# Performance work log

Measured on AMD Instinct MI355X. Metric: run time of the kernel, lower is better.

The kernel has to match this reference:

```python
import jax, jax.numpy as jnp
import numpy as np

TROPICAL_ZERO = jnp.float32(-1e38)  # tropical additive identity (acts as -inf)


def setup_inputs() -> dict:
    key = jax.random.key(0)
    k_x, k_w = jax.random.split(key)
    B, IN, OUT = 4096, 256, 256
    x = jax.random.normal(k_x, (B, IN), dtype=jnp.float32)
    # weight = log(rand + 1e-6), matching nn.Parameter init in the torch module
    weight = jnp.log(jax.random.uniform(k_w, (OUT, IN), dtype=jnp.float32) + 1e-6)
    bias = jnp.zeros((OUT,), dtype=jnp.float32)
    return {"x": x, "weight": weight, "bias": bias}


def reference(x, weight, bias):
    # Tropical (max-plus) matmul: out[b, j] = max_k (x[b, k] + w[j, k]) + bias[j]
    # restricted to 'non-tropical-zero' products; if all products are tropical
    # zero, the output stays TROPICAL_ZERO (no bias added), as in the torch loop.
    products = x[:, None, :] + weight[None, :, :]          # [B, out, in]
    mask = products > TROPICAL_ZERO                        # [B, out, in]
    masked = jnp.where(mask, products, -jnp.inf)
    max_val = jnp.max(masked, axis=-1)                     # [B, out]
    any_valid = jnp.any(mask, axis=-1)                     # [B, out]
    out = jnp.where(any_valid, max_val + bias[None, :], TROPICAL_ZERO)
    return out
```

## Files before the change

kernel.cpp:

```cpp
#include <hip/hip_runtime.h>


#define TZERO -1e38f

constexpr int Bdim = 4096;
constexpr int K    = 256;
constexpr int N    = 256;
constexpr int BM   = 64;
constexpr int BN   = 32;
constexpr int BK   = 32;
constexpr int XLD  = BM + 4;
constexpr int WLD  = BN + 4;
constexpr int NT   = 128;

__global__ __launch_bounds__(NT)
void tropical_kernel(const float* __restrict__ x, const float* __restrict__ w,
                     const float* __restrict__ bias, float* __restrict__ out)
{
    __shared__ float xs[BK][XLD];
    __shared__ float ws[BK][WLD];

    const int t    = threadIdx.x;
    const int tx   = t & 15;
    const int ty   = t >> 4;
    const int row0 = blockIdx.x * BM;
    const int col0 = blockIdx.y * BN;

    float acc[4][4];
#pragma unroll
    for (int i = 0; i < 4; ++i)
#pragma unroll
        for (int j = 0; j < 4; ++j)
            acc[i][j] = -__builtin_inff();

    for (int kc = 0; kc < K; kc += BK) {
#pragma unroll
        for (int i = 0; i < 4; ++i) {
            const int f  = t + i * NT;
            const int r  = f >> 3;
            const int k4 = f & 7;
            const float4 v = *reinterpret_cast<const float4*>(
                &x[(size_t)(row0 + r) * K + kc + k4 * 4]);
            xs[k4 * 4 + 0][r] = v.x;
            xs[k4 * 4 + 1][r] = v.y;
            xs[k4 * 4 + 2][r] = v.z;
            xs[k4 * 4 + 3][r] = v.w;
        }
#pragma unroll
        for (int i = 0; i < 2; ++i) {
            const int f  = t + i * NT;
            const int c  = f >> 3;
            const int k4 = f & 7;
            const float4 v = *reinterpret_cast<const float4*>(
                &w[(size_t)(col0 + c) * K + kc + k4 * 4]);
            ws[k4 * 4 + 0][c] = v.x;
            ws[k4 * 4 + 1][c] = v.y;
            ws[k4 * 4 + 2][c] = v.z;
            ws[k4 * 4 + 3][c] = v.w;
        }
        __syncthreads();

#pragma unroll
        for (int k = 0; k < BK; k += 2) {
            float xa[4], xb[4], wa[4], wb[4];
            *reinterpret_cast<float4*>(xa) =
                *reinterpret_cast<const float4*>(&xs[k][tx * 4]);
            *reinterpret_cast<float4*>(xb) =
                *reinterpret_cast<const float4*>(&xs[k + 1][tx * 4]);
            *reinterpret_cast<float4*>(wa) =
                *reinterpret_cast<const float4*>(&ws[k][ty * 4]);
            *reinterpret_cast<float4*>(wb) =
                *reinterpret_cast<const float4*>(&ws[k + 1][ty * 4]);
#pragma unroll
            for (int i = 0; i < 4; ++i)
#pragma unroll
                for (int j = 0; j < 4; ++j) {
                    const float t0 = xa[i] + wa[j];
                    const float t1 = xb[i] + wb[j];
                    acc[i][j] = fmaxf(fmaxf(acc[i][j], t0), t1);
                }
        }
        __syncthreads();
    }

    float bj[4];
    *reinterpret_cast<float4*>(bj) =
        *reinterpret_cast<const float4*>(&bias[col0 + ty * 4]);
#pragma unroll
    for (int i = 0; i < 4; ++i) {
        float4 o;
        o.x = (acc[i][0] > TZERO) ? acc[i][0] + bj[0] : TZERO;
        o.y = (acc[i][1] > TZERO) ? acc[i][1] + bj[1] : TZERO;
        o.z = (acc[i][2] > TZERO) ? acc[i][2] + bj[2] : TZERO;
        o.w = (acc[i][3] > TZERO) ? acc[i][3] + bj[3] : TZERO;
        *reinterpret_cast<float4*>(
            &out[(size_t)(row0 + tx * 4 + i) * N + col0 + ty * 4]) = o;
    }
}

extern "C" void kernel_launch(void* const* d_in, const int* in_sizes, int n_in,
                              void* d_out, int out_size, void* d_ws, size_t ws_size,
                              hipStream_t stream) {
    const float* x  = (const float*)d_in[0];
    const float* w  = (const float*)d_in[1];
    const float* b  = (const float*)d_in[2];
    float* out      = (float*)d_out;

    dim3 grid(Bdim / BM, N / BN);
    tropical_kernel<<<grid, NT, 0, stream>>>(x, w, b, out);
}
```

Measured before the change: 87.08 us.

## Restructure tropical matmul: full-K weight tile in LDS, x rows broadcast from global

Each block now stages a full 64-column by 256-K weight tile in shared memory as float4, and each wave handles 8 batch rows with one output column per lane. The x values are read straight from global memory with wave-uniform addresses, so every lane loads the same data as a broadcast. This removes the per-K-chunk LDS staging and its barriers, leaving a single sync. In exchange each lane computes only 8 outputs instead of 16, so arithmetic intensity per thread drops, and the 64KB LDS tile limits occupancy.

New measurement: 76.90 us. 11.7% less time.

```diff
diff --git a/kernel.cpp b/kernel.cpp
--- a/kernel.cpp
+++ b/kernel.cpp
@@ -3,98 +3,64 @@
 
 #define TZERO -1e38f
 
-constexpr int Bdim = 4096;
 constexpr int K    = 256;
 constexpr int N    = 256;
-constexpr int BM   = 64;
-constexpr int BN   = 32;
-constexpr int BK   = 32;
-constexpr int XLD  = BM + 4;
-constexpr int WLD  = BN + 4;
-constexpr int NT   = 128;
+constexpr int RPW  = 8;
+constexpr int WAVES = 4;
+constexpr int BM   = RPW * WAVES;
+constexpr int BN   = 64;
+constexpr int NT   = 64 * WAVES;
 
-__global__ __launch_bounds__(NT)
+__global__ __launch_bounds__(NT, 2)
 void tropical_kernel(const float* __restrict__ x, const float* __restrict__ w,
                      const float* __restrict__ bias, float* __restrict__ out)
 {
-    __shared__ float xs[BK][XLD];
-    __shared__ float ws[BK][WLD];
+    __shared__ float4 wQ[64][64];
 
     const int t    = threadIdx.x;
-    const int tx   = t & 15;
-    const int ty   = t >> 4;
     const int row0 = blockIdx.x * BM;
     const int col0 = blockIdx.y * BN;
 
-    float acc[4][4];
 #pragma unroll
-    for (int i = 0; i < 4; ++i)
+    for (int i = 0; i < (64 * 64) / NT; ++i) {
+        const int flat = t + i * NT;
+        const int j    = flat & 63;
+        const int k4   = flat >> 6;
+        wQ[k4][j] = *reinterpret_cast<const float4*>(
+            w + (size_t)(col0 + j) * K + k4 * 4);
+    }
+    __syncthreads();
+
+    const int lane = t & 63;
+    const int wave = __builtin_amdgcn_readfirstlane(t >> 6);
+    const float* xw = x + (size_t)(row0 + wave * RPW) * K;
+
+    float acc[RPW];
 #pragma unroll
-        for (int j = 0; j < 4; ++j)
-            acc[i][j] = -__builtin_inff();
+    for (int r = 0; r < RPW; ++r) acc[r] = -__builtin_inff();
 
-    for (int kc = 0; kc < K; kc += BK) {
+#pragma unroll 4
+    for (int k4 = 0; k4 < K / 4; ++k4) {
+        const float4 wv = wQ[k4][lane];
 #pragma unroll
-        for (int i = 0; i < 4; ++i) {
-            const int f  = t + i * NT;
-            const int r  = f >> 3;
-            const int k4 = f & 7;
-            const float4 v = *reinterpret_cast<const float4*>(
-                &x[(size_t)(row0 + r) * K + kc + k4 * 4]);
-            xs[k4 * 4 + 0][r] = v.x;
-            xs[k4 * 4 + 1][r] = v.y;
-            xs[k4 * 4 + 2][r] = v.z;
-            xs[k4 * 4 + 3][r] = v.w;
+        for (int r = 0; r < RPW; ++r) {
+            const float4 xv = *reinterpret_cast<const float4*>(xw + r * K + k4 * 4);
+            const float t0 = xv.x + wv.x;
+            const float t1 = xv.y + wv.y;
+            const float t2 = xv.z + wv.z;
+            const float t3 = xv.w + wv.w;
+            float m = fmaxf(fmaxf(acc[r], t0), t1);
+            m       = fmaxf(fmaxf(m, t2), t3);
+            acc[r] = m;
         }
-#pragma unroll
-        for (int i = 0; i < 2; ++i) {
-            const int f  = t + i * NT;
-            const int c  = f >> 3;
-            const int k4 = f & 7;
-            const float4 v = *reinterpret_cast<const float4*>(
-                &w[(size_t)(col0 + c) * K + kc + k4 * 4]);
-            ws[k4 * 4 + 0][c] = v.x;
-            ws[k4 * 4 + 1][c] = v.y;
-            ws[k4 * 4 + 2][c] = v.z;
-            ws[k4 * 4 + 3][c] = v.w;
-        }
-        __syncthreads();
-
-#pragma unroll
-        for (int k = 0; k < BK; k += 2) {
-            float xa[4], xb[4], wa[4], wb[4];
-            *reinterpret_cast<float4*>(xa) =
-                *reinterpret_cast<const float4*>(&xs[k][tx * 4]);
-            *reinterpret_cast<float4*>(xb) =
-                *reinterpret_cast<const float4*>(&xs[k + 1][tx * 4]);
-            *reinterpret_cast<float4*>(wa) =
-                *reinterpret_cast<const float4*>(&ws[k][ty * 4]);
-            *reinterpret_cast<float4*>(wb) =
-                *reinterpret_cast<const float4*>(&ws[k + 1][ty * 4]);
-#pragma unroll
-            for (int i = 0; i < 4; ++i)
-#pragma unroll
-                for (int j = 0; j < 4; ++j) {
-                    const float t0 = xa[i] + wa[j];
-                    const float t1 = xb[i] + wb[j];
-                    acc[i][j] = fmaxf(fmaxf(acc[i][j], t0), t1);
-                }
-        }
-        __syncthreads();
     }
 
-    float bj[4];
-    *reinterpret_cast<float4*>(bj) =
-        *reinterpret_cast<const float4*>(&bias[col0 + ty * 4]);
+    const float bj = bias[col0 + lane];
+    float* orow = out + (size_t)(row0 + wave * RPW) * N + col0 + lane;
 #pragma unroll
-    for (int i = 0; i < 4; ++i) {
-        float4 o;
-        o.x = (acc[i][0] > TZERO) ? acc[i][0] + bj[0] : TZERO;
-        o.y = (acc[i][1] > TZERO) ? acc[i][1] + bj[1] : TZERO;
-        o.z = (acc[i][2] > TZERO) ? acc[i][2] + bj[2] : TZERO;
-        o.w = (acc[i][3] > TZERO) ? acc[i][3] + bj[3] : TZERO;
-        *reinterpret_cast<float4*>(
-            &out[(size_t)(row0 + tx * 4 + i) * N + col0 + ty * 4]) = o;
+    for (int r = 0; r < RPW; ++r) {
+        const float v = acc[r];
+        orow[(size_t)r * N] = (v > TZERO) ? v + bj : TZERO;
     }
 }
 
@@ -106,6 +72,6 @@
     const float* b  = (const float*)d_in[2];
     float* out      = (float*)d_out;
 
-    dim3 grid(Bdim / BM, N / BN);
+    dim3 grid(4096 / BM, N / BN);
     tropical_kernel<<<grid, NT, 0, stream>>>(x, w, b, out);
 }
```
